# Kernel tuning notes

Measured on AMD Instinct MI355X. Metric: run time of the kernel, lower is better.

The kernel has to match this reference:

```python
import jax, jax.numpy as jnp
import numpy as np

CAPACITY = 0.125


def setup_inputs() -> dict:
    key = jax.random.key(0)
    ks = jax.random.split(key, 6)
    b, s, d, dff = 4, 8192, 512, 2048
    x = jax.random.normal(ks[0], (b, s, d), dtype=jnp.float32)
    position_ids = jnp.tile(jnp.arange(s, dtype=jnp.int64)[None, :], (b, 1))
    Wr = jax.random.normal(ks[1], (d,), dtype=jnp.float32) * 0.02
    br = jnp.zeros((1,), dtype=jnp.float32)
    W1 = jax.random.normal(ks[2], (d, dff), dtype=jnp.float32) * 0.02
    b1 = jnp.zeros((dff,), dtype=jnp.float32)
    W2 = jax.random.normal(ks[3], (dff, d), dtype=jnp.float32) * 0.02
    b2 = jnp.zeros((d,), dtype=jnp.float32)
    return {"x": x, "position_ids": position_ids, "Wr": Wr, "br": br,
            "W1": W1, "b1": b1, "W2": W2, "b2": b2}


def reference(x, position_ids, Wr, br, W1, b1, W2, b2):
    b, s, d = x.shape
    # Router: Linear(d, 1) -> squeeze(-1)
    weights = jnp.einsum('bsd,d->bs', x, Wr) + br  # [b, s]
    k = int(CAPACITY * s)
    # Per-batch top-k threshold (k-th largest value)
    top_k_values = jax.lax.top_k(weights, k)[0]  # [b, k], sorted desc
    threshold = top_k_values[:, -1]              # [b]
    selected_mask = weights > threshold[:, None]  # strict >, ties excluded (matches torch)
    # Block: per-token MLP (Linear-GELU-Linear). Per-token ops commute with the
    # gather/scatter, so computing densely and masking is mathematically identical
    # to the original gather -> block -> weighted scatter.
    h = jax.nn.gelu(jnp.einsum('bsd,df->bsf', x, W1) + b1)
    y = jnp.einsum('bsf,fd->bsd', h, W2) + b2
    # processed_tokens (= block_out * router_weight on selected) + x on unselected
    out = jnp.where(selected_mask[..., None], y * weights[..., None], x)
    return out
```

## Files before the change

kernel.cpp:

```cpp
#include <hip/hip_runtime.h>
#include <hip/hip_bf16.h>

#define B_   4
#define S_   8192
#define D_   512
#define DFF_ 2048
#define K_TOP 1024

typedef unsigned short u16;
typedef __attribute__((ext_vector_type(8))) short bf16x8;
typedef __attribute__((ext_vector_type(4))) float floatx4;

__device__ __forceinline__ unsigned f2key(float f){
    unsigned u = __float_as_uint(f);
    return (u & 0x80000000u) ? ~u : (u | 0x80000000u);
}
__device__ __forceinline__ u16 f2b(float f){
    unsigned u = __float_as_uint(f);
    u = (u + 0x7FFFu + ((u >> 16) & 1u)) >> 16;
    return (u16)u;
}
__device__ __forceinline__ float gelu_fast(float v){
    float u = 1.5957691216f * v + 0.0713548162726f * v * v * v;
    float e = __expf(u);
    return v - v / (e + 1.0f);
}
__device__ __forceinline__ void gl_lds16(const void* gptr, void* lptr){
    auto g = (const __attribute__((address_space(1))) unsigned int*)((uintptr_t)gptr);
    auto l = (__attribute__((address_space(3))) unsigned int*)((uintptr_t)lptr);
    __builtin_amdgcn_global_load_lds(g, l, 16, 0, 0);
}


__global__ __launch_bounds__(256) void prep_kernel(
    const float* __restrict__ W1, const float* __restrict__ W2,
    u16* __restrict__ W1t, u16* __restrict__ W2t,
    const float4* __restrict__ x,
    const float4* __restrict__ Wr4, const float* __restrict__ br,
    float* __restrict__ w_all, unsigned* __restrict__ ghist)
{
    __shared__ __align__(16) unsigned char shmem[128 * 132 * 2];
    const int tid = threadIdx.x;
    const int bx = blockIdx.x;
    if (bx < 128){
        const float* src; u16* dst; int R, C, ct, ks;
        if (bx < 64){ src = W1; dst = W1t; R = D_;   C = DFF_; ct = bx & 15;        ks = bx >> 4; }
        else        { src = W2; dst = W2t; R = DFF_; C = D_;   ct = (bx - 64) & 3;  ks = (bx - 64) >> 2; }
        u16 (*tile)[132] = (u16(*)[132])shmem;
        #pragma unroll
        for (int it = 0; it < 64; it++){
            int lin = it * 256 + tid;
            int kk = lin >> 7, nn = lin & 127;
            tile[kk][nn] = f2b(src[(size_t)(ks * 128 + kk) * C + ct * 128 + nn]);
        }
        __syncthreads();
        u16* base = dst + (size_t)(ct * (R / 128) + ks) * 16384;
        const int r = tid >> 1, h = tid & 1;
        #pragma unroll
        for (int c = 0; c < 8; c++){
            int cl = h * 8 + c;
            bf16x8 bv;
            #pragma unroll
            for (int e = 0; e < 8; e++) bv[e] = (short)tile[cl * 8 + e][r];
            *(bf16x8*)&base[r * 128 + ((cl ^ (r & 15)) << 3)] = bv;
        }
    } else {
        unsigned* hist = (unsigned*)shmem;
        if (tid < 256) hist[tid] = 0u;
        __syncthreads();
        const int wb = bx - 128;
        const int wv = tid >> 6, lane = tid & 63;
        const int t0 = wb * 64 + wv * 16;
        const float brv = br[0];
        const float4 wr0 = Wr4[lane], wr1 = Wr4[lane + 64];
        #pragma unroll
        for (int g = 0; g < 4; g++){
            float a[4];
            #pragma unroll
            for (int tt = 0; tt < 4; tt++){
                const float4* xt = x + (size_t)(t0 + g * 4 + tt) * 128;
                float4 v0 = xt[lane], v1 = xt[lane + 64];
                a[tt] = v0.x*wr0.x + v0.y*wr0.y + v0.z*wr0.z + v0.w*wr0.w
                      + v1.x*wr1.x + v1.y*wr1.y + v1.z*wr1.z + v1.w*wr1.w;
            }
            #pragma unroll
            for (int off = 32; off > 0; off >>= 1){
                #pragma unroll
                for (int tt = 0; tt < 4; tt++) a[tt] += __shfl_down(a[tt], off, 64);
            }
            if (lane == 0){
                #pragma unroll
                for (int tt = 0; tt < 4; tt++){
                    float wt = a[tt] + brv;
                    w_all[t0 + g * 4 + tt] = wt;
                    atomicAdd(&hist[f2key(wt) >> 24], 1u);
                }
            }
        }
        __syncthreads();
        if (tid < 256) ghist[wb * 256 + tid] = hist[tid];
    }
}

__global__ __launch_bounds__(1024) void kth_compact_kernel(
    const float4* __restrict__ w_all4, const unsigned* __restrict__ ghist,
    int* __restrict__ counts, unsigned* __restrict__ thr_out,
    int* __restrict__ idx)
{
    __shared__ unsigned keys[S_];
    __shared__ unsigned hist[4][256];
    __shared__ unsigned sprefix;
    __shared__ int sremk;
    __shared__ int lbase;
    const int b = blockIdx.x, tid = threadIdx.x;
    const int wv = tid >> 6, lane = tid & 63;
    const float4* row4 = w_all4 + (size_t)b * (S_ / 4);

    #pragma unroll
    for (int i = 0; i < 2; i++){
        int j = tid + i * 1024;
        float4 v = row4[j];
        keys[4*j+0] = f2key(v.x); keys[4*j+1] = f2key(v.y);
        keys[4*j+2] = f2key(v.z); keys[4*j+3] = f2key(v.w);
    }
    {
        const int bin = tid & 255, q = tid >> 8;
        unsigned s = 0;
        const unsigned* gh = ghist + (size_t)(b * 128 + q * 32) * 256 + bin;
        #pragma unroll 8
        for (int j = 0; j < 32; j++) s += gh[j * 256];
        hist[q][bin] = s;
    }
    if (tid == 0){ sprefix = 0u; sremk = K_TOP; lbase = 0; }
    __syncthreads();

    for (int pass = 3; pass >= 0; pass--){
        const int shift = pass * 8;
        if (pass < 3){
            ((unsigned*)hist)[tid] = 0u;
            __syncthreads();
            const unsigned mask_hi = 0xFFFFFFFFu << (shift + 8);
            const unsigned pfx = sprefix;
            #pragma unroll
            for (int i = 0; i < 8; i++){
                unsigned key = keys[tid + i * 1024];
                if ((key & mask_hi) == pfx)
                    atomicAdd(&hist[wv & 3][(key >> shift) & 255u], 1u);
            }
            __syncthreads();
        }
        if (wv == 0){
            const unsigned remk = (unsigned)sremk;
            const unsigned pfx = sprefix;
            unsigned c[4];
            #pragma unroll
            for (int q = 0; q < 4; q++)
                c[q] = hist[0][4*lane+q] + hist[1][4*lane+q]
                     + hist[2][4*lane+q] + hist[3][4*lane+q];
            unsigned t = c[0] + c[1] + c[2] + c[3];
            unsigned ss = t;
            #pragma unroll
            for (int off = 1; off < 64; off <<= 1){
                unsigned o = __shfl_down(ss, off, 64);
                ss += (lane + off < 64) ? o : 0u;
            }
            const unsigned sgt = ss - t;
            unsigned suf[4];
            suf[3] = c[3] + sgt; suf[2] = c[2] + suf[3];
            suf[1] = c[1] + suf[2]; suf[0] = c[0] + suf[1];
            #pragma unroll
            for (int q = 0; q < 4; q++){
                unsigned nx = suf[q] - c[q];
                if (suf[q] >= remk && nx < remk){
                    sprefix = pfx | ((unsigned)(4 * lane + q) << shift);
                    sremk = (int)(remk - nx);
                }
            }
        }
        __syncthreads();
    }

    const unsigned thr = sprefix;
    #pragma unroll
    for (int i = 0; i < 8; i++){
        int li = tid + i * 1024;
        bool sel = keys[li] > thr;
        unsigned long long m = __ballot(sel);
        int wtot = (int)__popcll(m);
        if (wtot){
            int woff = 0;
            if (lane == 0) woff = atomicAdd(&lbase, wtot);
            woff = __shfl(woff, 0, 64);
            if (sel){
                int pos = woff + (int)__popcll(m & ((1ull << lane) - 1ull));
                idx[b * 1024 + pos] = b * S_ + li;
            }
        }
    }
    __syncthreads();
    if (tid == 0){ counts[b] = lbase; thr_out[b] = thr; }
}

__global__ __launch_bounds__(256) void gather_kernel(
    const float* __restrict__ x, const int* __restrict__ idx,
    const int* __restrict__ counts, u16* __restrict__ XbT)
{
    const int mt = blockIdx.x, s = blockIdx.y;
    const int cl = threadIdx.x & 15, r16 = threadIdx.x >> 4;
    u16* base = XbT + (size_t)(mt * 4 + s) * 16384;
    #pragma unroll
    for (int it = 0; it < 8; it++){
        int r = r16 + it * 16;
        int mg = mt * 128 + r;
        if ((mg & 1023) < counts[mg >> 10]){
            const float* xp = x + (size_t)idx[mg] * D_ + s * 128 + cl * 8;
            float4 v0 = *(const float4*)xp;
            float4 v1 = *(const float4*)(xp + 4);
            bf16x8 bv;
            bv[0]=(short)f2b(v0.x); bv[1]=(short)f2b(v0.y);
            bv[2]=(short)f2b(v0.z); bv[3]=(short)f2b(v0.w);
            bv[4]=(short)f2b(v1.x); bv[5]=(short)f2b(v1.y);
            bv[6]=(short)f2b(v1.z); bv[7]=(short)f2b(v1.w);
            *(bf16x8*)&base[r * 128 + ((cl ^ (r & 15)) << 3)] = bv;
        }
    }
}

__device__ __forceinline__ void copy_unselected(
    const float4* __restrict__ x, float4* __restrict__ out,
    const float* __restrict__ w_all, const unsigned* __restrict__ thr,
    int cIdx, int tid)
{
    const int wv = tid >> 6, lane = tid & 63;
    const int tBase = cIdx * 128 + wv * 32;
    #pragma unroll 2
    for (int tt = 0; tt < 32; tt++){
        int t = tBase + tt;
        float wt = w_all[t];
        if (f2key(wt) <= thr[t >> 13]){
            const float4* xs = x + (size_t)t * 128;
            float4* od = out + (size_t)t * 128;
            od[lane]      = xs[lane];
            od[lane + 64] = xs[lane + 64];
        }
    }
}

__global__ __launch_bounds__(256) void ffn1_kernel(
    const u16* __restrict__ XbT, const u16* __restrict__ W1t,
    const int* __restrict__ counts, const float* __restrict__ bias1,
    u16* __restrict__ Ht,
    const float4* __restrict__ x, float4* __restrict__ out,
    const float* __restrict__ w_all, const unsigned* __restrict__ thr)
{
    __shared__ __align__(16) u16 smem[32768];
    const int tid = threadIdx.x;
    const int bx = blockIdx.x;
    if (bx >= 512){
        copy_unselected(x, out, w_all, thr, bx - 512, tid);
        return;
    }
    const int mBlk = bx & 31, nBlk = bx >> 5;
    const int lane = tid & 63, w = tid >> 6;
    const int wr = (w >> 1) * 64, wc = (w & 1) * 64;
    const int fr = lane & 15, quad = lane >> 4;

    const char* Abase = (const char*)(XbT + (size_t)mBlk * 4 * 16384);
    const char* Bbase = (const char*)(W1t + (size_t)nBlk * 4 * 16384);
    char* Al0 = (char*)smem + tid * 16;
    char* Bl0 = (char*)(smem + 16384) + tid * 16;
    const int rr0 = tid >> 3, pp = tid & 7;

    auto stage = [&](const char* gbase, char* lb, int hs){
        const char* s0 = gbase + (size_t)(hs >> 1) * 32768;
        const int h = hs & 1;
        #pragma unroll
        for (int i = 0; i < 4; i++){
            int r = rr0 + i * 32;
            int pg = pp | (((h ^ (r >> 3)) & 1) << 3);
            gl_lds16(s0 + r * 256 + pg * 16, lb + i * 4096);
        }
    };

    stage(Abase, Al0, 0);
    stage(Bbase, Bl0, 0);

    floatx4 acc[4][4] = {};
    for (int hs = 0; hs < 8; hs++){
        __builtin_amdgcn_s_barrier();
        if (hs + 1 < 8){
            stage(Abase, Al0 + ((hs + 1) & 1) * 16384, hs + 1);
            stage(Bbase, Bl0 + ((hs + 1) & 1) * 16384, hs + 1);
            asm volatile("s_waitcnt vmcnt(8)" ::: "memory");
        } else {
            asm volatile("s_waitcnt vmcnt(0)" ::: "memory");
        }
        __builtin_amdgcn_sched_barrier(0);
        __builtin_amdgcn_s_barrier();
        const u16* Ab = smem + (hs & 1) * 8192;
        const u16* Bb = smem + 16384 + (hs & 1) * 8192;
        __builtin_amdgcn_s_setprio(1);
        #pragma unroll
        for (int ks2 = 0; ks2 < 2; ks2++){
            bf16x8 af[4], bf[4];
            #pragma unroll
            for (int i = 0; i < 4; i++){
                int r = wr + i * 16 + fr;
                af[i] = *(const bf16x8*)&Ab[r * 64 + (((ks2 * 4 + quad) ^ (r & 7)) << 3)];
            }
            #pragma unroll
            for (int j = 0; j < 4; j++){
                int r = wc + j * 16 + fr;
                bf[j] = *(const bf16x8*)&Bb[r * 64 + (((ks2 * 4 + quad) ^ (r & 7)) << 3)];
            }
            #pragma unroll
            for (int i = 0; i < 4; i++)
                #pragma unroll
                for (int j = 0; j < 4; j++)
                    acc[i][j] = __builtin_amdgcn_mfma_f32_16x16x32_bf16(af[i], bf[j], acc[i][j], 0, 0, 0);
        }
        __builtin_amdgcn_s_setprio(0);
    }

    float bj[4];
    #pragma unroll
    for (int j = 0; j < 4; j++) bj[j] = bias1[nBlk * 128 + wc + j * 16 + fr];

    __syncthreads();
    u16* Cs = smem;
    #pragma unroll
    for (int i = 0; i < 4; i++){
        #pragma unroll
        for (int rg = 0; rg < 4; rg++){
            int r = wr + i * 16 + quad * 4 + rg;
            #pragma unroll
            for (int j = 0; j < 4; j++){
                int col = wc + j * 16 + fr;
                float v = gelu_fast(acc[i][j][rg] + bj[j]);
                Cs[r * 128 + ((((col >> 3) ^ (r & 15)) << 3) | (col & 7))] = f2b(v);
            }
        }
    }
    __syncthreads();
    const int r = tid >> 1, h = tid & 1;
    int mg = mBlk * 128 + r;
    if ((mg & 1023) < counts[mg >> 10]){
        u16* dstp = Ht + (((size_t)(mBlk * 2 + (r >> 6)) * 16 + nBlk) * 64 + (r & 63)) * 128;
        #pragma unroll
        for (int p = 0; p < 8; p++){
            int pc = h * 8 + p;
            *(bf16x8*)&dstp[pc << 3] = *(const bf16x8*)&Cs[r * 128 + (pc << 3)];
        }
    }
}

__global__ __launch_bounds__(256) void ffn2_kernel(
    const u16* __restrict__ Ht, const u16* __restrict__ W2t,
    const int* __restrict__ counts, const int* __restrict__ idx,
    const float* __restrict__ w_all, const float* __restrict__ bias2,
    float* __restrict__ out,
    const float4* __restrict__ x, const unsigned* __restrict__ thr)
{
    __shared__ __align__(16) u16 smem[24576];
    const int tid = threadIdx.x;
    const int bx = blockIdx.x;
    if (bx >= 256){
        copy_unselected(x, (float4*)out, w_all, thr, 128 + (bx - 256), tid);
        return;
    }
    const int mBlk = bx & 63, nBlk = bx >> 6;
    const int lane = tid & 63, w = tid >> 6;
    const int wr = (w >> 1) * 32, wc = (w & 1) * 64;
    const int fr = lane & 15, quad = lane >> 4;

    const char* Abase = (const char*)(Ht + (size_t)mBlk * 16 * 8192);
    const char* Bbase = (const char*)(W2t + (size_t)nBlk * 16 * 16384);
    char* Al0 = (char*)smem + tid * 16;
    char* Bl0 = (char*)(smem + 8192) + tid * 16;
    const int rr0 = tid >> 3, pp = tid & 7;

    auto stage = [&](int buf, int hs){
        const int h = hs & 1;
        {
            const char* s0 = Abase + (size_t)(hs >> 1) * 16384;
            char* l = Al0 + buf * 8192;
            #pragma unroll
            for (int i = 0; i < 2; i++){
                int r = rr0 + i * 32;
                int pg = pp | (((h ^ (r >> 3)) & 1) << 3);
                gl_lds16(s0 + r * 256 + pg * 16, l + i * 4096);
            }
        }
        {
            const char* s0 = Bbase + (size_t)(hs >> 1) * 32768;
            char* l = Bl0 + buf * 16384;
            #pragma unroll
            for (int i = 0; i < 4; i++){
                int r = rr0 + i * 32;
                int pg = pp | (((h ^ (r >> 3)) & 1) << 3);
                gl_lds16(s0 + r * 256 + pg * 16, l + i * 4096);
            }
        }
    };

    stage(0, 0);
    floatx4 acc[2][4] = {};
    for (int hs = 0; hs < 32; hs++){
        __builtin_amdgcn_s_barrier();
        if (hs + 1 < 32){
            stage((hs + 1) & 1, hs + 1);
            asm volatile("s_waitcnt vmcnt(6)" ::: "memory");
        } else {
            asm volatile("s_waitcnt vmcnt(0)" ::: "memory");
        }
        __builtin_amdgcn_sched_barrier(0);
        __builtin_amdgcn_s_barrier();
        const u16* Ab = smem + (hs & 1) * 4096;
        const u16* Bb = smem + 8192 + (hs & 1) * 8192;
        __builtin_amdgcn_s_setprio(1);
        #pragma unroll
        for (int ks2 = 0; ks2 < 2; ks2++){
            bf16x8 af[2], bf[4];
            #pragma unroll
            for (int i = 0; i < 2; i++){
                int r = wr + i * 16 + fr;
                af[i] = *(const bf16x8*)&Ab[r * 64 + (((ks2 * 4 + quad) ^ (r & 7)) << 3)];
            }
            #pragma unroll
            for (int j = 0; j < 4; j++){
                int r = wc + j * 16 + fr;
                bf[j] = *(const bf16x8*)&Bb[r * 64 + (((ks2 * 4 + quad) ^ (r & 7)) << 3)];
            }
            #pragma unroll
            for (int i = 0; i < 2; i++)
                #pragma unroll
                for (int j = 0; j < 4; j++)
                    acc[i][j] = __builtin_amdgcn_mfma_f32_16x16x32_bf16(af[i], bf[j], acc[i][j], 0, 0, 0);
        }
        __builtin_amdgcn_s_setprio(0);
    }

    float bj[4];
    #pragma unroll
    for (int j = 0; j < 4; j++) bj[j] = bias2[nBlk * 128 + wc + j * 16 + fr];

    __syncthreads();
    float* Cs = (float*)smem;
    #pragma unroll
    for (int i = 0; i < 2; i++){
        #pragma unroll
        for (int rg = 0; rg < 4; rg++){
            int r = wr + i * 16 + quad * 4 + rg;
            #pragma unroll
            for (int j = 0; j < 4; j++)
                Cs[r * 128 + wc + j * 16 + fr] = acc[i][j][rg] + bj[j];
        }
    }
    __syncthreads();
    const int r = tid >> 2, q = tid & 3;
    int mg = mBlk * 64 + r;
    if ((mg & 1023) < counts[mg >> 10]){
        int token = idx[mg];
        float wt = w_all[token];
        float* op = out + (size_t)token * D_ + nBlk * 128 + q * 32;
        const float4* cp = (const float4*)&Cs[r * 128 + q * 32];
        #pragma unroll
        for (int p = 0; p < 8; p++){
            float4 vv = cp[p];
            vv.x *= wt; vv.y *= wt; vv.z *= wt; vv.w *= wt;
            ((float4*)op)[p] = vv;
        }
    }
}

extern "C" void kernel_launch(void* const* d_in, const int* in_sizes, int n_in,
                              void* d_out, int out_size, void* d_ws, size_t ws_size,
                              hipStream_t stream)
{
    const float* x  = (const float*)d_in[0];
    const float* Wr = (const float*)d_in[2];
    const float* br = (const float*)d_in[3];
    const float* W1 = (const float*)d_in[4];
    const float* b1 = (const float*)d_in[5];
    const float* W2 = (const float*)d_in[6];
    const float* b2 = (const float*)d_in[7];
    float* out = (float*)d_out;
    char* ws = (char*)d_ws;

    float*    w_all  = (float*)   (ws + 0);
    int*      counts = (int*)     (ws + 131072);
    unsigned* thr    = (unsigned*)(ws + 131088);
    int*      idx    = (int*)     (ws + 131136);
    unsigned* ghist  = (unsigned*)(ws + 163840);
    u16*      XbT    = (u16*)     (ws + 720896);
    u16*      W1t    = (u16*)     (ws + 4915200);
    u16*      W2t    = (u16*)     (ws + 7012352);
    u16*      Ht     = (u16*)     (ws + 9109504);

    prep_kernel<<<640, 256, 0, stream>>>(
        W1, W2, W1t, W2t, (const float4*)x,
        (const float4*)Wr, br, w_all, ghist);
    kth_compact_kernel<<<B_, 1024, 0, stream>>>(
        (const float4*)w_all, ghist, counts, thr, idx);
    gather_kernel<<<dim3(32, 4), 256, 0, stream>>>(x, idx, counts, XbT);
    ffn1_kernel<<<640, 256, 0, stream>>>(
        XbT, W1t, counts, b1, Ht, (const float4*)x, (float4*)out, w_all, thr);
    ffn2_kernel<<<384, 256, 0, stream>>>(
        Ht, W2t, counts, idx, w_all, b2, out, (const float4*)x, thr);
}
```

Baseline: 197.0 us.

## Fuse pipeline into a persistent cooperative megakernel with grid syncs

```diff
diff --git a/kernel.cpp b/kernel.cpp
--- a/kernel.cpp
+++ b/kernel.cpp
@@ -1,5 +1,8 @@
 #include <hip/hip_runtime.h>
 #include <hip/hip_bf16.h>
+#include <hip/hip_cooperative_groups.h>
+
+namespace cg = cooperative_groups;
 
 #define B_   4
 #define S_   8192
@@ -32,126 +35,78 @@
 }
 
 
-__global__ __launch_bounds__(256) void prep_kernel(
-    const float* __restrict__ W1, const float* __restrict__ W2,
-    u16* __restrict__ W1t, u16* __restrict__ W2t,
-    const float4* __restrict__ x,
+__device__ __forceinline__ void phase_router(int bx, int tid,
+    const float4* __restrict__ x, float4* __restrict__ out,
     const float4* __restrict__ Wr4, const float* __restrict__ br,
-    float* __restrict__ w_all, unsigned* __restrict__ ghist)
-{
-    __shared__ __align__(16) unsigned char shmem[128 * 132 * 2];
-    const int tid = threadIdx.x;
-    const int bx = blockIdx.x;
-    if (bx < 128){
-        const float* src; u16* dst; int R, C, ct, ks;
-        if (bx < 64){ src = W1; dst = W1t; R = D_;   C = DFF_; ct = bx & 15;        ks = bx >> 4; }
-        else        { src = W2; dst = W2t; R = DFF_; C = D_;   ct = (bx - 64) & 3;  ks = (bx - 64) >> 2; }
-        u16 (*tile)[132] = (u16(*)[132])shmem;
-        #pragma unroll
-        for (int it = 0; it < 64; it++){
-            int lin = it * 256 + tid;
-            int kk = lin >> 7, nn = lin & 127;
-            tile[kk][nn] = f2b(src[(size_t)(ks * 128 + kk) * C + ct * 128 + nn]);
-        }
-        __syncthreads();
-        u16* base = dst + (size_t)(ct * (R / 128) + ks) * 16384;
-        const int r = tid >> 1, h = tid & 1;
-        #pragma unroll
-        for (int c = 0; c < 8; c++){
-            int cl = h * 8 + c;
-            bf16x8 bv;
-            #pragma unroll
-            for (int e = 0; e < 8; e++) bv[e] = (short)tile[cl * 8 + e][r];
-            *(bf16x8*)&base[r * 128 + ((cl ^ (r & 15)) << 3)] = bv;
-        }
-    } else {
-        unsigned* hist = (unsigned*)shmem;
-        if (tid < 256) hist[tid] = 0u;
-        __syncthreads();
-        const int wb = bx - 128;
-        const int wv = tid >> 6, lane = tid & 63;
-        const int t0 = wb * 64 + wv * 16;
-        const float brv = br[0];
-        const float4 wr0 = Wr4[lane], wr1 = Wr4[lane + 64];
-        #pragma unroll
-        for (int g = 0; g < 4; g++){
-            float a[4];
-            #pragma unroll
-            for (int tt = 0; tt < 4; tt++){
-                const float4* xt = x + (size_t)(t0 + g * 4 + tt) * 128;
-                float4 v0 = xt[lane], v1 = xt[lane + 64];
-                a[tt] = v0.x*wr0.x + v0.y*wr0.y + v0.z*wr0.z + v0.w*wr0.w
-                      + v1.x*wr1.x + v1.y*wr1.y + v1.z*wr1.z + v1.w*wr1.w;
-            }
-            #pragma unroll
-            for (int off = 32; off > 0; off >>= 1){
-                #pragma unroll
-                for (int tt = 0; tt < 4; tt++) a[tt] += __shfl_down(a[tt], off, 64);
-            }
-            if (lane == 0){
-                #pragma unroll
-                for (int tt = 0; tt < 4; tt++){
-                    float wt = a[tt] + brv;
-                    w_all[t0 + g * 4 + tt] = wt;
-                    atomicAdd(&hist[f2key(wt) >> 24], 1u);
-                }
-            }
-        }
-        __syncthreads();
-        if (tid < 256) ghist[wb * 256 + tid] = hist[tid];
-    }
-}
-
-__global__ __launch_bounds__(1024) void kth_compact_kernel(
-    const float4* __restrict__ w_all4, const unsigned* __restrict__ ghist,
-    int* __restrict__ counts, unsigned* __restrict__ thr_out,
+    float* __restrict__ w_all)
+{
+    const int wv = tid >> 6, lane = tid & 63;
+    const int t0 = bx * 64 + wv * 16;
+    const float brv = br[0];
+    const float4 wr0 = Wr4[lane], wr1 = Wr4[lane + 64];
+    #pragma unroll
+    for (int g = 0; g < 4; g++){
+        float a[4];
+        #pragma unroll
+        for (int tt = 0; tt < 4; tt++){
+            const int t = t0 + g * 4 + tt;
+            const float4* xt = x + (size_t)t * 128;
+            float4* ot = out + (size_t)t * 128;
+            float4 v0 = xt[lane], v1 = xt[lane + 64];
+            ot[lane] = v0; ot[lane + 64] = v1;
+            a[tt] = v0.x*wr0.x + v0.y*wr0.y + v0.z*wr0.z + v0.w*wr0.w
+                  + v1.x*wr1.x + v1.y*wr1.y + v1.z*wr1.z + v1.w*wr1.w;
+        }
+        #pragma unroll
+        for (int off = 32; off > 0; off >>= 1){
+            #pragma unroll
+            for (int tt = 0; tt < 4; tt++) a[tt] += __shfl_down(a[tt], off, 64);
+        }
+        if (lane == 0){
+            #pragma unroll
+            for (int tt = 0; tt < 4; tt++) w_all[t0 + g * 4 + tt] = a[tt] + brv;
+        }
+    }
+}
+
+__device__ __forceinline__ void phase_kth(char* shm, int b, int tid,
+    const float4* __restrict__ w_all4, int* __restrict__ counts,
     int* __restrict__ idx)
 {
-    __shared__ unsigned keys[S_];
-    __shared__ unsigned hist[4][256];
-    __shared__ unsigned sprefix;
-    __shared__ int sremk;
-    __shared__ int lbase;
-    const int b = blockIdx.x, tid = threadIdx.x;
+    unsigned* keys = (unsigned*)shm;
+    unsigned (*hist)[256] = (unsigned(*)[256])(shm + 32768);
+    unsigned* sprefix = (unsigned*)(shm + 36864);
+    int* sremk = (int*)(shm + 36872);
+    int* lbase = (int*)(shm + 36880);
     const int wv = tid >> 6, lane = tid & 63;
     const float4* row4 = w_all4 + (size_t)b * (S_ / 4);
 
     #pragma unroll
-    for (int i = 0; i < 2; i++){
-        int j = tid + i * 1024;
+    for (int i = 0; i < 8; i++){
+        int j = tid + i * 256;
         float4 v = row4[j];
         keys[4*j+0] = f2key(v.x); keys[4*j+1] = f2key(v.y);
         keys[4*j+2] = f2key(v.z); keys[4*j+3] = f2key(v.w);
     }
-    {
-        const int bin = tid & 255, q = tid >> 8;
-        unsigned s = 0;
-        const unsigned* gh = ghist + (size_t)(b * 128 + q * 32) * 256 + bin;
-        #pragma unroll 8
-        for (int j = 0; j < 32; j++) s += gh[j * 256];
-        hist[q][bin] = s;
-    }
-    if (tid == 0){ sprefix = 0u; sremk = K_TOP; lbase = 0; }
+    if (tid == 0){ *sprefix = 0u; *sremk = K_TOP; *lbase = 0; }
     __syncthreads();
 
     for (int pass = 3; pass >= 0; pass--){
         const int shift = pass * 8;
-        if (pass < 3){
-            ((unsigned*)hist)[tid] = 0u;
-            __syncthreads();
-            const unsigned mask_hi = 0xFFFFFFFFu << (shift + 8);
-            const unsigned pfx = sprefix;
-            #pragma unroll
-            for (int i = 0; i < 8; i++){
-                unsigned key = keys[tid + i * 1024];
-                if ((key & mask_hi) == pfx)
-                    atomicAdd(&hist[wv & 3][(key >> shift) & 255u], 1u);
-            }
-            __syncthreads();
-        }
+        #pragma unroll
+        for (int i = 0; i < 4; i++) ((unsigned*)hist)[tid + i * 256] = 0u;
+        __syncthreads();
+        const unsigned mask_hi = (pass == 3) ? 0u : (0xFFFFFFFFu << (shift + 8));
+        const unsigned pfx = *sprefix;
+        #pragma unroll 8
+        for (int i = 0; i < 32; i++){
+            unsigned key = keys[tid + i * 256];
+            if ((key & mask_hi) == pfx)
+                atomicAdd(&hist[wv][(key >> shift) & 255u], 1u);
+        }
+        __syncthreads();
         if (wv == 0){
-            const unsigned remk = (unsigned)sremk;
-            const unsigned pfx = sprefix;
+            const unsigned remk = (unsigned)*sremk;
             unsigned c[4];
             #pragma unroll
             for (int q = 0; q < 4; q++)
@@ -172,24 +127,24 @@
             for (int q = 0; q < 4; q++){
                 unsigned nx = suf[q] - c[q];
                 if (suf[q] >= remk && nx < remk){
-                    sprefix = pfx | ((unsigned)(4 * lane + q) << shift);
-                    sremk = (int)(remk - nx);
+                    *sprefix = pfx | ((unsigned)(4 * lane + q) << shift);
+                    *sremk = (int)(remk - nx);
                 }
             }
         }
         __syncthreads();
     }
 
-    const unsigned thr = sprefix;
-    #pragma unroll
-    for (int i = 0; i < 8; i++){
-        int li = tid + i * 1024;
+    const unsigned thr = *sprefix;
+    #pragma unroll 8
+    for (int i = 0; i < 32; i++){
+        int li = tid + i * 256;
         bool sel = keys[li] > thr;
         unsigned long long m = __ballot(sel);
         int wtot = (int)__popcll(m);
         if (wtot){
             int woff = 0;
-            if (lane == 0) woff = atomicAdd(&lbase, wtot);
+            if (lane == 0) woff = atomicAdd(lbase, wtot);
             woff = __shfl(woff, 0, 64);
             if (sel){
                 int pos = woff + (int)__popcll(m & ((1ull << lane) - 1ull));
@@ -198,19 +153,46 @@
         }
     }
     __syncthreads();
-    if (tid == 0){ counts[b] = lbase; thr_out[b] = thr; }
-}
-
-__global__ __launch_bounds__(256) void gather_kernel(
+    if (tid == 0) counts[b] = *lbase;
+}
+
+__device__ __forceinline__ void phase_conv(char* shm, int cv, int tid,
+    const float* __restrict__ W1, const float* __restrict__ W2,
+    u16* __restrict__ W1t, u16* __restrict__ W2t)
+{
+    const float* src; u16* dst; int R, C, ct, ks;
+    if (cv < 64){ src = W1; dst = W1t; R = D_;   C = DFF_; ct = cv & 15;        ks = cv >> 4; }
+    else        { src = W2; dst = W2t; R = DFF_; C = D_;   ct = (cv - 64) & 3;  ks = (cv - 64) >> 2; }
+    u16 (*tile)[132] = (u16(*)[132])shm;
+    #pragma unroll
+    for (int it = 0; it < 64; it++){
+        int lin = it * 256 + tid;
+        int kk = lin >> 7, nn = lin & 127;
+        tile[kk][nn] = f2b(src[(size_t)(ks * 128 + kk) * C + ct * 128 + nn]);
+    }
+    __syncthreads();
+    u16* base = dst + (size_t)(ct * (R / 128) + ks) * 16384;
+    const int r = tid >> 1, h = tid & 1;
+    #pragma unroll
+    for (int c = 0; c < 8; c++){
+        int cl = h * 8 + c;
+        bf16x8 bv;
+        #pragma unroll
+        for (int e = 0; e < 8; e++) bv[e] = (short)tile[cl * 8 + e][r];
+        *(bf16x8*)&base[r * 128 + ((cl ^ (r & 15)) << 3)] = bv;
+    }
+}
+
+__device__ __forceinline__ void phase_gather(int bx, int tid,
     const float* __restrict__ x, const int* __restrict__ idx,
     const int* __restrict__ counts, u16* __restrict__ XbT)
 {
-    const int mt = blockIdx.x, s = blockIdx.y;
-    const int cl = threadIdx.x & 15, r16 = threadIdx.x >> 4;
+    const int mt = bx >> 4, s = (bx >> 2) & 3, q = bx & 3;
+    const int cl = tid & 15, r16 = tid >> 4;
     u16* base = XbT + (size_t)(mt * 4 + s) * 16384;
     #pragma unroll
-    for (int it = 0; it < 8; it++){
-        int r = r16 + it * 16;
+    for (int it = 0; it < 2; it++){
+        int r = q * 32 + r16 + it * 16;
         int mg = mt * 128 + r;
         if ((mg & 1023) < counts[mg >> 10]){
             const float* xp = x + (size_t)idx[mg] * D_ + s * 128 + cl * 8;
@@ -226,49 +208,22 @@
     }
 }
 
-__device__ __forceinline__ void copy_unselected(
-    const float4* __restrict__ x, float4* __restrict__ out,
-    const float* __restrict__ w_all, const unsigned* __restrict__ thr,
-    int cIdx, int tid)
-{
-    const int wv = tid >> 6, lane = tid & 63;
-    const int tBase = cIdx * 128 + wv * 32;
-    #pragma unroll 2
-    for (int tt = 0; tt < 32; tt++){
-        int t = tBase + tt;
-        float wt = w_all[t];
-        if (f2key(wt) <= thr[t >> 13]){
-            const float4* xs = x + (size_t)t * 128;
-            float4* od = out + (size_t)t * 128;
-            od[lane]      = xs[lane];
-            od[lane + 64] = xs[lane + 64];
-        }
-    }
-}
-
-__global__ __launch_bounds__(256) void ffn1_kernel(
+__device__ __forceinline__ void phase_ffn1(char* shm, int bx, int tid,
     const u16* __restrict__ XbT, const u16* __restrict__ W1t,
     const int* __restrict__ counts, const float* __restrict__ bias1,
-    u16* __restrict__ Ht,
-    const float4* __restrict__ x, float4* __restrict__ out,
-    const float* __restrict__ w_all, const unsigned* __restrict__ thr)
-{
-    __shared__ __align__(16) u16 smem[32768];
-    const int tid = threadIdx.x;
-    const int bx = blockIdx.x;
-    if (bx >= 512){
-        copy_unselected(x, out, w_all, thr, bx - 512, tid);
-        return;
-    }
-    const int mBlk = bx & 31, nBlk = bx >> 5;
+    u16* __restrict__ Ht)
+{
+    const int task = (bx & 7) * 64 + (bx >> 3);
+    const int mBlk = task & 31, nBlk = task >> 5;
     const int lane = tid & 63, w = tid >> 6;
     const int wr = (w >> 1) * 64, wc = (w & 1) * 64;
     const int fr = lane & 15, quad = lane >> 4;
+    u16* smem = (u16*)shm;
 
     const char* Abase = (const char*)(XbT + (size_t)mBlk * 4 * 16384);
     const char* Bbase = (const char*)(W1t + (size_t)nBlk * 4 * 16384);
-    char* Al0 = (char*)smem + tid * 16;
-    char* Bl0 = (char*)(smem + 16384) + tid * 16;
+    char* Al0 = shm + tid * 16;
+    char* Bl0 = shm + 32768 + tid * 16;
     const int rr0 = tid >> 3, pp = tid & 7;
 
     auto stage = [&](const char* gbase, char* lb, int hs){
@@ -281,7 +236,6 @@
             gl_lds16(s0 + r * 256 + pg * 16, lb + i * 4096);
         }
     };
-
     stage(Abase, Al0, 0);
     stage(Bbase, Bl0, 0);
 
@@ -354,106 +308,88 @@
     }
 }
 
-__global__ __launch_bounds__(256) void ffn2_kernel(
+__device__ __forceinline__ void phase_ffn2(char* shm, int bx, int tid,
     const u16* __restrict__ Ht, const u16* __restrict__ W2t,
     const int* __restrict__ counts, const int* __restrict__ idx,
     const float* __restrict__ w_all, const float* __restrict__ bias2,
-    float* __restrict__ out,
-    const float4* __restrict__ x, const unsigned* __restrict__ thr)
-{
-    __shared__ __align__(16) u16 smem[24576];
-    const int tid = threadIdx.x;
-    const int bx = blockIdx.x;
-    if (bx >= 256){
-        copy_unselected(x, (float4*)out, w_all, thr, 128 + (bx - 256), tid);
-        return;
-    }
-    const int mBlk = bx & 63, nBlk = bx >> 6;
+    float* __restrict__ out)
+{
+    const int task = (bx & 7) * 64 + (bx >> 3);
+    const int mBlk = task & 63, nCol = task >> 6;
     const int lane = tid & 63, w = tid >> 6;
-    const int wr = (w >> 1) * 32, wc = (w & 1) * 64;
+    const int wr = (w >> 1) * 32, wc = (w & 1) * 32;
     const int fr = lane & 15, quad = lane >> 4;
-
-    const char* Abase = (const char*)(Ht + (size_t)mBlk * 16 * 8192);
-    const char* Bbase = (const char*)(W2t + (size_t)nBlk * 16 * 16384);
-    char* Al0 = (char*)smem + tid * 16;
-    char* Bl0 = (char*)(smem + 8192) + tid * 16;
-    const int rr0 = tid >> 3, pp = tid & 7;
-
-    auto stage = [&](int buf, int hs){
-        const int h = hs & 1;
-        {
-            const char* s0 = Abase + (size_t)(hs >> 1) * 16384;
-            char* l = Al0 + buf * 8192;
-            #pragma unroll
-            for (int i = 0; i < 2; i++){
-                int r = rr0 + i * 32;
-                int pg = pp | (((h ^ (r >> 3)) & 1) << 3);
-                gl_lds16(s0 + r * 256 + pg * 16, l + i * 4096);
-            }
-        }
-        {
-            const char* s0 = Bbase + (size_t)(hs >> 1) * 32768;
-            char* l = Bl0 + buf * 16384;
-            #pragma unroll
-            for (int i = 0; i < 4; i++){
-                int r = rr0 + i * 32;
-                int pg = pp | (((h ^ (r >> 3)) & 1) << 3);
-                gl_lds16(s0 + r * 256 + pg * 16, l + i * 4096);
-            }
+    u16* smem = (u16*)shm;
+
+    const char* Abase = (const char*)Ht + (size_t)mBlk * 262144;
+    const char* Bbase = (const char*)W2t + (size_t)(nCol >> 1) * 16 * 32768
+                                         + (size_t)(nCol & 1) * 16384;
+    char* Al0 = shm + tid * 16;
+    char* Bl0 = shm + 32768 + tid * 16;
+
+    auto stage2 = [&](int buf, int ks){
+        const char* ga = Abase + (size_t)ks * 16384 + tid * 16;
+        const char* gb = Bbase + (size_t)ks * 32768 + tid * 16;
+        char* la = Al0 + buf * 16384;
+        char* lb = Bl0 + buf * 16384;
+        #pragma unroll
+        for (int i = 0; i < 4; i++){
+            gl_lds16(ga + i * 4096, la + i * 4096);
+            gl_lds16(gb + i * 4096, lb + i * 4096);
         }
     };
-
-    stage(0, 0);
-    floatx4 acc[2][4] = {};
-    for (int hs = 0; hs < 32; hs++){
+    stage2(0, 0);
+
+    floatx4 acc[2][2] = {};
+    for (int ks = 0; ks < 16; ks++){
         __builtin_amdgcn_s_barrier();
-        if (hs + 1 < 32){
-            stage((hs + 1) & 1, hs + 1);
-            asm volatile("s_waitcnt vmcnt(6)" ::: "memory");
+        if (ks + 1 < 16){
+            stage2((ks + 1) & 1, ks + 1);
+            asm volatile("s_waitcnt vmcnt(8)" ::: "memory");
         } else {
             asm volatile("s_waitcnt vmcnt(0)" ::: "memory");
         }
         __builtin_amdgcn_sched_barrier(0);
         __builtin_amdgcn_s_barrier();
-        const u16* Ab = smem + (hs & 1) * 4096;
-        const u16* Bb = smem + 8192 + (hs & 1) * 8192;
+        const u16* Ab = smem + (ks & 1) * 8192;
+        const u16* Bb = smem + 16384 + (ks & 1) * 8192;
         __builtin_amdgcn_s_setprio(1);
         #pragma unroll
-        for (int ks2 = 0; ks2 < 2; ks2++){
-            bf16x8 af[2], bf[4];
+        for (int ks2 = 0; ks2 < 4; ks2++){
+            bf16x8 af[2], bf[2];
             #pragma unroll
             for (int i = 0; i < 2; i++){
                 int r = wr + i * 16 + fr;
-                af[i] = *(const bf16x8*)&Ab[r * 64 + (((ks2 * 4 + quad) ^ (r & 7)) << 3)];
-            }
-            #pragma unroll
-            for (int j = 0; j < 4; j++){
+                af[i] = *(const bf16x8*)&Ab[r * 128 + (((ks2 * 4 + quad) ^ (r & 15)) << 3)];
+            }
+            #pragma unroll
+            for (int j = 0; j < 2; j++){
                 int r = wc + j * 16 + fr;
-                bf[j] = *(const bf16x8*)&Bb[r * 64 + (((ks2 * 4 + quad) ^ (r & 7)) << 3)];
+                bf[j] = *(const bf16x8*)&Bb[r * 128 + (((ks2 * 4 + quad) ^ (r & 15)) << 3)];
             }
             #pragma unroll
             for (int i = 0; i < 2; i++)
                 #pragma unroll
-                for (int j = 0; j < 4; j++)
+                for (int j = 0; j < 2; j++)
                     acc[i][j] = __builtin_amdgcn_mfma_f32_16x16x32_bf16(af[i], bf[j], acc[i][j], 0, 0, 0);
         }
         __builtin_amdgcn_s_setprio(0);
     }
 
-    float bj[4];
-    #pragma unroll
-    for (int j = 0; j < 4; j++) bj[j] = bias2[nBlk * 128 + wc + j * 16 + fr];
-
-    __syncthreads();
-    float* Cs = (float*)smem;
+    float bj[2];
+    #pragma unroll
+    for (int j = 0; j < 2; j++) bj[j] = bias2[nCol * 64 + wc + j * 16 + fr];
+
+    __syncthreads();
+    float* Cs = (float*)shm;
     #pragma unroll
     for (int i = 0; i < 2; i++){
         #pragma unroll
         for (int rg = 0; rg < 4; rg++){
             int r = wr + i * 16 + quad * 4 + rg;
             #pragma unroll
-            for (int j = 0; j < 4; j++)
-                Cs[r * 128 + wc + j * 16 + fr] = acc[i][j][rg] + bj[j];
+            for (int j = 0; j < 2; j++)
+                Cs[r * 64 + wc + j * 16 + fr] = acc[i][j][rg] + bj[j];
         }
     }
     __syncthreads();
@@ -462,15 +398,73 @@
     if ((mg & 1023) < counts[mg >> 10]){
         int token = idx[mg];
         float wt = w_all[token];
-        float* op = out + (size_t)token * D_ + nBlk * 128 + q * 32;
-        const float4* cp = (const float4*)&Cs[r * 128 + q * 32];
-        #pragma unroll
-        for (int p = 0; p < 8; p++){
+        float* op = out + (size_t)token * D_ + nCol * 64 + q * 16;
+        const float4* cp = (const float4*)&Cs[r * 64 + q * 16];
+        #pragma unroll
+        for (int p = 0; p < 4; p++){
             float4 vv = cp[p];
             vv.x *= wt; vv.y *= wt; vv.z *= wt; vv.w *= wt;
             ((float4*)op)[p] = vv;
         }
     }
+}
+
+__global__ __launch_bounds__(256, 2) void mega_kernel(
+    const float* x, const float* Wr, const float* br,
+    const float* W1, const float* b1, const float* W2, const float* b2,
+    float* out, float* w_all, int* counts, int* idx,
+    u16* XbT, u16* W1t, u16* W2t, u16* Ht)
+{
+    __shared__ __align__(16) char shm[65536];
+    cg::grid_group grid = cg::this_grid();
+    const int bx = blockIdx.x, tid = threadIdx.x;
+
+    phase_router(bx, tid, (const float4*)x, (float4*)out,
+                 (const float4*)Wr, br, w_all);
+    grid.sync();
+    if (bx < 4)        phase_kth(shm, bx, tid, (const float4*)w_all, counts, idx);
+    else if (bx < 132) phase_conv(shm, bx - 4, tid, W1, W2, W1t, W2t);
+    grid.sync();
+    phase_gather(bx, tid, x, idx, counts, XbT);
+    grid.sync();
+    phase_ffn1(shm, bx, tid, XbT, W1t, counts, b1, Ht);
+    grid.sync();
+    phase_ffn2(shm, bx, tid, Ht, W2t, counts, idx, w_all, b2, out);
+}
+
+__global__ __launch_bounds__(256) void k_router(
+    const float* x, float* out, const float* Wr, const float* br, float* w_all)
+{
+    phase_router(blockIdx.x, threadIdx.x, (const float4*)x, (float4*)out,
+                 (const float4*)Wr, br, w_all);
+}
+__global__ __launch_bounds__(256) void k_kthconv(
+    const float* w_all, int* counts, int* idx,
+    const float* W1, const float* W2, u16* W1t, u16* W2t)
+{
+    __shared__ __align__(16) char shm[65536];
+    if (blockIdx.x < 4)
+        phase_kth(shm, blockIdx.x, threadIdx.x, (const float4*)w_all, counts, idx);
+    else
+        phase_conv(shm, blockIdx.x - 4, threadIdx.x, W1, W2, W1t, W2t);
+}
+__global__ __launch_bounds__(256) void k_gather(
+    const float* x, const int* idx, const int* counts, u16* XbT)
+{
+    phase_gather(blockIdx.x, threadIdx.x, x, idx, counts, XbT);
+}
+__global__ __launch_bounds__(256) void k_ffn1(
+    const u16* XbT, const u16* W1t, const int* counts, const float* b1, u16* Ht)
+{
+    __shared__ __align__(16) char shm[65536];
+    phase_ffn1(shm, blockIdx.x, threadIdx.x, XbT, W1t, counts, b1, Ht);
+}
+__global__ __launch_bounds__(256) void k_ffn2(
+    const u16* Ht, const u16* W2t, const int* counts, const int* idx,
+    const float* w_all, const float* b2, float* out)
+{
+    __shared__ __align__(16) char shm[65536];
+    phase_ffn2(shm, blockIdx.x, threadIdx.x, Ht, W2t, counts, idx, w_all, b2, out);
 }
 
 extern "C" void kernel_launch(void* const* d_in, const int* in_sizes, int n_in,
@@ -487,24 +481,27 @@
     float* out = (float*)d_out;
     char* ws = (char*)d_ws;
 
-    float*    w_all  = (float*)   (ws + 0);
-    int*      counts = (int*)     (ws + 131072);
-    unsigned* thr    = (unsigned*)(ws + 131088);
-    int*      idx    = (int*)     (ws + 131136);
-    unsigned* ghist  = (unsigned*)(ws + 163840);
-    u16*      XbT    = (u16*)     (ws + 720896);
-    u16*      W1t    = (u16*)     (ws + 4915200);
-    u16*      W2t    = (u16*)     (ws + 7012352);
-    u16*      Ht     = (u16*)     (ws + 9109504);
-
-    prep_kernel<<<640, 256, 0, stream>>>(
-        W1, W2, W1t, W2t, (const float4*)x,
-        (const float4*)Wr, br, w_all, ghist);
-    kth_compact_kernel<<<B_, 1024, 0, stream>>>(
-        (const float4*)w_all, ghist, counts, thr, idx);
-    gather_kernel<<<dim3(32, 4), 256, 0, stream>>>(x, idx, counts, XbT);
-    ffn1_kernel<<<640, 256, 0, stream>>>(
-        XbT, W1t, counts, b1, Ht, (const float4*)x, (float4*)out, w_all, thr);
-    ffn2_kernel<<<384, 256, 0, stream>>>(
-        Ht, W2t, counts, idx, w_all, b2, out, (const float4*)x, thr);
-}
+    float* w_all  = (float*)(ws + 0);
+    int*   counts = (int*)  (ws + 131072);
+    int*   idx    = (int*)  (ws + 131136);
+    u16*   XbT    = (u16*)  (ws + 262144);
+    u16*   W1t    = (u16*)  (ws + 4456448);
+    u16*   W2t    = (u16*)  (ws + 6553600);
+    u16*   Ht     = (u16*)  (ws + 8650752);
+
+    void* args[] = {
+        (void*)&x, (void*)&Wr, (void*)&br, (void*)&W1, (void*)&b1,
+        (void*)&W2, (void*)&b2, (void*)&out, (void*)&w_all,
+        (void*)&counts, (void*)&idx, (void*)&XbT, (void*)&W1t,
+        (void*)&W2t, (void*)&Ht };
+
+    hipError_t e = hipLaunchCooperativeKernel((const void*)mega_kernel,
+                       dim3(512), dim3(256), args, 0, stream);
+    if (e != hipSuccess){
+        k_router <<<512, 256, 0, stream>>>(x, out, Wr, br, w_all);
+        k_kthconv<<<132, 256, 0, stream>>>(w_all, counts, idx, W1, W2, W1t, W2t);
+        k_gather <<<512, 256, 0, stream>>>(x, idx, counts, XbT);
+        k_ffn1   <<<512, 256, 0, stream>>>(XbT, W1t, counts, b1, Ht);
+        k_ffn2   <<<512, 256, 0, stream>>>(Ht, W2t, counts, idx, w_all, b2, out);
+    }
+}
```

Measured after the change: 443.9 us. +125.3%, slower.
